# Kernel optimization log

Hardware: AMD Instinct MI355X
Metric: run time of the kernel (lower is better)

The kernel has to match this reference:

```python
import math
import jax, jax.numpy as jnp
import numpy as np

INPUT_DIM = 1024
OUTPUT_DIM = 1024
DEGREE = 8
EPS = 1.0


def setup_inputs() -> dict:
    key = jax.random.key(0)
    k1, k2 = jax.random.split(key)
    x = jax.random.normal(k1, (8192, INPUT_DIM), dtype=jnp.float32)
    std = 1.0 / (INPUT_DIM * (DEGREE + 1))
    hermite_coeffs = std * jax.random.normal(k2, (INPUT_DIM, OUTPUT_DIM, DEGREE + 1), dtype=jnp.float32)
    return {"x": x, "hermite_coeffs": hermite_coeffs}


def _hermite_basis(x):
    # x: [B, I] squashed input; returns [B, I, DEGREE+1] Hermite-function basis.
    pi_q = math.pi ** (-0.25)
    gauss = jnp.exp(-0.5 * x * x)
    h0 = pi_q * gauss
    hs = [h0]
    if DEGREE > 0:
        hs.append(math.sqrt(2.0) * pi_q * x * gauss)
    for i in range(2, DEGREE + 1):
        hs.append(math.sqrt(2.0 / i) * x * hs[i - 1] - math.sqrt((i - 1) / i) * hs[i - 2])
    return jnp.stack(hs, axis=-1)


def reference(x, hermite_coeffs):
    x = x.reshape(-1, INPUT_DIM)
    x = jnp.tanh(x) * (math.sqrt(2 * DEGREE + 1) + EPS)
    hermite = _hermite_basis(x)  # [B, I, D+1]
    y = jnp.einsum('bid,iod->bo', hermite, hermite_coeffs)
    return y.reshape(-1, OUTPUT_DIM)
```

## Files before the change

kernel.cpp:

```cpp
#include <hip/hip_runtime.h>

#define MDIM 8192
#define IDIM 1024
#define ODIM 1024
#define D1   9
#define KDIM (IDIM * D1)

typedef _Float16 half8   __attribute__((ext_vector_type(8)));
typedef _Float16 half2v  __attribute__((ext_vector_type(2)));
typedef float    float4v __attribute__((ext_vector_type(4)));

#define BSCALE 256.0f
#define INV_BSCALE (1.0f / 256.0f)
#define USCALE 5.123105625617661f
#define H0C 0.7511255444649425f
#define SQRT2 1.4142135623730951f

__device__ __forceinline__ void hermite9(float xv, float h[D1]) {
    float ax = fabsf(xv);
    float t  = __expf(-2.0f * ax);
    float th = (1.0f - t) / (1.0f + t);
    th = copysignf(th, xv);
    float u = th * USCALE;
    float g = __expf(-0.5f * u * u);
    h[0] = H0C * g;
    h[1] = SQRT2 * H0C * u * g;
    const float c1[D1] = {0.f, 0.f, 1.0f, 0.8164965809277260f, 0.7071067811865476f,
                          0.6324555320336759f, 0.5773502691896258f, 0.5345224838248488f, 0.5f};
    const float c2[D1] = {0.f, 0.f, 0.7071067811865476f, 0.8164965809277260f, 0.8660254037844386f,
                          0.8944271909999159f, 0.9128709291752769f, 0.9258200997725514f, 0.9354143466934853f};
#pragma unroll
    for (int d = 2; d < D1; ++d) h[d] = c1[d] * u * h[d - 1] - c2[d] * h[d - 2];
}

__global__ __launch_bounds__(256) void prep_b(const float* __restrict__ C,
                                              _Float16* __restrict__ Bt) {
    __shared__ float lds[288 * 33];
    const int t  = threadIdx.x;
    const int ti = blockIdx.x & 31;
    const int to = blockIdx.x >> 5;
    const float* base = C + (size_t)ti * 32 * 9216 + (size_t)to * 32 * 9;
#pragma unroll
    for (int j = 0; j < 36; ++j) {
        int f   = t + 256 * j;
        int row = f / 288;
        int col = f - row * 288;
        lds[col * 33 + row] = base[(size_t)row * 9216 + col];
    }
    __syncthreads();
    _Float16* bb = Bt + (size_t)to * 32 * KDIM + ti * 32;
#pragma unroll
    for (int j = 0; j < 36; ++j) {
        int e   = t + 256 * j;
        int i   = e & 31;
        int odp = e >> 5;
        int ol  = odp / 9;
        int d   = odp - ol * 9;
        bb[(size_t)ol * KDIM + d * IDIM + i] = (_Float16)(lds[odp * 33 + i] * BSCALE);
    }
}

__global__ __launch_bounds__(256) void prep_u(const float* __restrict__ x,
                                              _Float16* __restrict__ U,
                                              _Float16* __restrict__ H0) {
    size_t t = (size_t)blockIdx.x * 256 + threadIdx.x;
    const float4* xp = (const float4*)(x + t * 8);
    float4 a0 = xp[0], a1 = xp[1];
    float xv[8] = {a0.x, a0.y, a0.z, a0.w, a1.x, a1.y, a1.z, a1.w};
    half8 uu, hh;
#pragma unroll
    for (int e = 0; e < 8; ++e) {
        float v  = xv[e];
        float t2 = __expf(-2.0f * fabsf(v));
        float th = (1.0f - t2) / (1.0f + t2);
        float u  = copysignf(th, v) * USCALE;
        float g  = __expf(-0.5f * u * u);
        uu[e] = (_Float16)u;
        hh[e] = (_Float16)(H0C * g);
    }
    *(half8*)(U  + t * 8) = uu;
    *(half8*)(H0 + t * 8) = hh;
}

__global__ __launch_bounds__(256, 2) void gemm_fused2(
    const _Float16* __restrict__ U,
    const _Float16* __restrict__ H0,
    const _Float16* __restrict__ Bt,
    float* __restrict__ out)
{
    const int tid = threadIdx.x;
    const int w = tid >> 6;
    const int l = tid & 63;
    const int bn = blockIdx.x;
    const int bm = blockIdx.y;

    __shared__ _Float16 As[2][128 * 64];
    __shared__ _Float16 Bs[2][128 * 64];

    const int lrow8 = l >> 3;
    const int kgrp  = (l & 7) ^ lrow8;
    const _Float16* Bg = Bt + ((size_t)(bn * 128 + w * 8 + lrow8) * KDIM + kgrp * 8);

    const int q   = l >> 4;
    const int m16 = l & 15;
    const int s3  = m16 & 7;
    const int wm  = w >> 1, wn = w & 1;

    const int r  = tid >> 1;
    const int ih = tid & 1;
    const int r7 = r & 7;
    const size_t urow = (((size_t)(bm * 128 + r)) << 10) + ih * 32;

    constexpr float c1a[D1] = {0.f, 0.f, 1.0f, 0.8164965809277260f, 0.7071067811865476f,
                               0.6324555320336759f, 0.5773502691896258f, 0.5345224838248488f, 0.5f};
    constexpr float c2a[D1] = {0.f, 0.f, 0.7071067811865476f, 0.8164965809277260f, 0.8660254037844386f,
                               0.8944271909999159f, 0.9128709291752769f, 0.9258200997725514f, 0.9354143466934853f};

    half2v u2[16], hA[16], hB[16];
    const half2v sq2 = half2v{(_Float16)SQRT2, (_Float16)SQRT2};

    auto loadUH = [&](int kb) {
        const half8* up = (const half8*)(U  + urow + kb);
        const half8* hp = (const half8*)(H0 + urow + kb);
        half8 ub[4], hb[4];
#pragma unroll
        for (int a = 0; a < 4; ++a) { ub[a] = up[a]; hb[a] = hp[a]; }
#pragma unroll
        for (int a = 0; a < 4; ++a)
#pragma unroll
            for (int b = 0; b < 4; ++b) {
                u2[4*a+b] = half2v{ub[a][2*b], ub[a][2*b+1]};
                hA[4*a+b] = half2v{hb[a][2*b], hb[a][2*b+1]};
            }
#pragma unroll
        for (int p = 0; p < 16; ++p) hB[p] = sq2 * u2[p] * hA[p];
    };

    _Float16* arow0 = &As[0][r * 64];
    _Float16* arow1 = &As[1][r * 64];
    auto writeA = [&](int buf, const half2v ht[16]) {
        _Float16* arow = buf ? arow1 : arow0;
#pragma unroll
        for (int c = 0; c < 4; ++c) {
            int slot = (ih * 4 + c) ^ r7;
            half8 vv;
#pragma unroll
            for (int pp = 0; pp < 4; ++pp) {
                vv[2*pp+0] = ht[4*c+pp][0];
                vv[2*pp+1] = ht[4*c+pp][1];
            }
            *(half8*)(arow + slot * 8) = vv;
        }
    };

    float4v acc[4][4] = {};

#pragma unroll
    for (int rr = 0; rr < 4; ++rr)
        __builtin_amdgcn_global_load_lds(
            (const __attribute__((address_space(1))) void*)(Bg + (size_t)(rr * 32) * KDIM),
            (__attribute__((address_space(3))) void*)((char*)&Bs[0][0] + (rr * 4 + w) * 1024),
            16, 0, 0);
    loadUH(0);
    writeA(0, hA);
    __syncthreads();

    for (int ib = 0; ib < 16; ++ib) {
        const int kbase = ib * 64;
#pragma unroll
        for (int d = 0; d < D1; ++d) {
            const int cur = (ib + d) & 1;
            const int nxt = cur ^ 1;
            const bool has_next = (d < 8) || (ib < 15);

            if (has_next) {
                const int nkoff = (d == 8) ? (kbase + 64)
                                           : ((d + 1) * IDIM + kbase);
#pragma unroll
                for (int rr = 0; rr < 4; ++rr)
                    __builtin_amdgcn_global_load_lds(
                        (const __attribute__((address_space(1))) void*)(Bg + (size_t)(rr * 32) * KDIM + nkoff),
                        (__attribute__((address_space(3))) void*)((char*)&Bs[nxt][0] + (rr * 4 + w) * 1024),
                        16, 0, 0);
            }

            half2v ht[16];
            if (has_next) {
                if (d == 8) {
                    loadUH(kbase + 64);
#pragma unroll
                    for (int p = 0; p < 16; ++p) ht[p] = hA[p];
                } else if (d == 0) {
#pragma unroll
                    for (int p = 0; p < 16; ++p) ht[p] = hB[p];
                } else {
                    const half2v c1v = half2v{(_Float16)c1a[d+1], (_Float16)c1a[d+1]};
                    const half2v c2v = half2v{(_Float16)c2a[d+1], (_Float16)c2a[d+1]};
#pragma unroll
                    for (int p = 0; p < 16; ++p) {
                        half2v t = u2[p] * hB[p];
                        ht[p] = c1v * t - c2v * hA[p];
                        hA[p] = hB[p];
                        hB[p] = ht[p];
                    }
                }
            }

#pragma unroll
            for (int ko = 0; ko < 2; ++ko) {
                const int slot = (q + 4 * ko) ^ s3;
                half8 af[4], bf[4];
#pragma unroll
                for (int i = 0; i < 4; ++i) {
                    af[i] = *(const half8*)&As[cur][(wm * 64 + i * 16 + m16) * 64 + slot * 8];
                    bf[i] = *(const half8*)&Bs[cur][(wn * 64 + i * 16 + m16) * 64 + slot * 8];
                }
#pragma unroll
                for (int i = 0; i < 4; ++i)
#pragma unroll
                    for (int j = 0; j < 4; ++j)
                        acc[i][j] = __builtin_amdgcn_mfma_f32_16x16x32_f16(af[i], bf[j], acc[i][j], 0, 0, 0);
            }

            if (has_next) writeA(nxt, ht);

            __syncthreads();
        }
    }

#pragma unroll
    for (int i = 0; i < 4; ++i) {
        int row = bm * 128 + wm * 64 + i * 16 + q * 4;
#pragma unroll
        for (int j = 0; j < 4; ++j) {
            int col = bn * 128 + wn * 64 + j * 16 + m16;
            float* op = out + (size_t)row * ODIM + col;
#pragma unroll
            for (int r2 = 0; r2 < 4; ++r2)
                op[(size_t)r2 * ODIM] = acc[i][j][r2] * INV_BSCALE;
        }
    }
}

__global__ void naive_kernel(const float* __restrict__ x, const float* __restrict__ C,
                             float* __restrict__ out) {
    __shared__ float hb[IDIM * D1];
    int b = blockIdx.x;
    int tid = threadIdx.x;
    for (int i = tid; i < IDIM; i += 256) {
        float h[D1];
        hermite9(x[(size_t)b * IDIM + i], h);
#pragma unroll
        for (int d = 0; d < D1; ++d) hb[i * D1 + d] = h[d];
    }
    __syncthreads();
    for (int o = tid; o < ODIM; o += 256) {
        float acc = 0.f;
        for (int i = 0; i < IDIM; ++i) {
            const float* cp = C + ((size_t)i * ODIM + o) * D1;
            const float* hp = hb + i * D1;
#pragma unroll
            for (int d = 0; d < D1; ++d) acc += hp[d] * cp[d];
        }
        out[(size_t)b * ODIM + o] = acc;
    }
}

extern "C" void kernel_launch(void* const* d_in, const int* in_sizes, int n_in,
                              void* d_out, int out_size, void* d_ws, size_t ws_size,
                              hipStream_t stream) {
    const float* x      = (const float*)d_in[0];
    const float* coeffs = (const float*)d_in[1];
    float* out = (float*)d_out;

    const size_t bt_bytes = (size_t)ODIM * KDIM * sizeof(_Float16);
    const size_t u_bytes  = (size_t)MDIM * IDIM * sizeof(_Float16);

    if (ws_size >= bt_bytes + 2 * u_bytes) {
        _Float16* Bt = (_Float16*)d_ws;
        _Float16* Uv = (_Float16*)((char*)d_ws + bt_bytes);
        _Float16* H0 = (_Float16*)((char*)d_ws + bt_bytes + u_bytes);
        hipLaunchKernelGGL(prep_b, dim3(1024), dim3(256), 0, stream, coeffs, Bt);
        hipLaunchKernelGGL(prep_u, dim3((MDIM * IDIM) / 2048), dim3(256), 0, stream, x, Uv, H0);
        hipLaunchKernelGGL(gemm_fused2, dim3(8, 64), dim3(256), 0, stream, Uv, H0, Bt, out);
    } else {
        hipLaunchKernelGGL(naive_kernel, dim3(MDIM), dim3(256), 0, stream, x, coeffs, out);
    }
}
```

Before: 281.1 us.

## Generate Hermite A-fragments in registers per wave and merge prep kernels

The GEMM no longer builds the Hermite A tile in shared memory. Each wave loads U and H0 straight into its MFMA fragment layout and runs the recurrence in registers as packed half8 ops, which removes the A LDS writes and reads and halves LDS use. The two prep kernels are merged into one launch, and the tanh divide becomes a reciprocal. In exchange, each wave recomputes the recurrence for its 64 rows (done twice across wn waves), reads U/H0 redundantly from global, and uses more registers, which may limit occupancy.

```diff
diff --git a/kernel.cpp b/kernel.cpp
--- a/kernel.cpp
+++ b/kernel.cpp
@@ -7,7 +7,6 @@
 #define KDIM (IDIM * D1)
 
 typedef _Float16 half8   __attribute__((ext_vector_type(8)));
-typedef _Float16 half2v  __attribute__((ext_vector_type(2)));
 typedef float    float4v __attribute__((ext_vector_type(4)));
 
 #define BSCALE 256.0f
@@ -15,6 +14,11 @@
 #define USCALE 5.123105625617661f
 #define H0C 0.7511255444649425f
 #define SQRT2 1.4142135623730951f
+
+__device__ __forceinline__ half8 splat8(float f) {
+    _Float16 h = (_Float16)f;
+    return half8{h, h, h, h, h, h, h, h};
+}
 
 __device__ __forceinline__ void hermite9(float xv, float h[D1]) {
     float ax = fabsf(xv);
@@ -33,56 +37,57 @@
     for (int d = 2; d < D1; ++d) h[d] = c1[d] * u * h[d - 1] - c2[d] * h[d - 2];
 }
 
-__global__ __launch_bounds__(256) void prep_b(const float* __restrict__ C,
-                                              _Float16* __restrict__ Bt) {
-    __shared__ float lds[288 * 33];
-    const int t  = threadIdx.x;
-    const int ti = blockIdx.x & 31;
-    const int to = blockIdx.x >> 5;
-    const float* base = C + (size_t)ti * 32 * 9216 + (size_t)to * 32 * 9;
-#pragma unroll
-    for (int j = 0; j < 36; ++j) {
-        int f   = t + 256 * j;
-        int row = f / 288;
-        int col = f - row * 288;
-        lds[col * 33 + row] = base[(size_t)row * 9216 + col];
-    }
-    __syncthreads();
-    _Float16* bb = Bt + (size_t)to * 32 * KDIM + ti * 32;
-#pragma unroll
-    for (int j = 0; j < 36; ++j) {
-        int e   = t + 256 * j;
-        int i   = e & 31;
-        int odp = e >> 5;
-        int ol  = odp / 9;
-        int d   = odp - ol * 9;
-        bb[(size_t)ol * KDIM + d * IDIM + i] = (_Float16)(lds[odp * 33 + i] * BSCALE);
-    }
-}
-
-__global__ __launch_bounds__(256) void prep_u(const float* __restrict__ x,
-                                              _Float16* __restrict__ U,
-                                              _Float16* __restrict__ H0) {
-    size_t t = (size_t)blockIdx.x * 256 + threadIdx.x;
-    const float4* xp = (const float4*)(x + t * 8);
-    float4 a0 = xp[0], a1 = xp[1];
-    float xv[8] = {a0.x, a0.y, a0.z, a0.w, a1.x, a1.y, a1.z, a1.w};
-    half8 uu, hh;
-#pragma unroll
-    for (int e = 0; e < 8; ++e) {
-        float v  = xv[e];
-        float t2 = __expf(-2.0f * fabsf(v));
-        float th = (1.0f - t2) / (1.0f + t2);
-        float u  = copysignf(th, v) * USCALE;
-        float g  = __expf(-0.5f * u * u);
-        uu[e] = (_Float16)u;
-        hh[e] = (_Float16)(H0C * g);
-    }
-    *(half8*)(U  + t * 8) = uu;
-    *(half8*)(H0 + t * 8) = hh;
-}
-
-__global__ __launch_bounds__(256, 2) void gemm_fused2(
+__global__ __launch_bounds__(256) void prep_all(const float* __restrict__ C,
+                                                _Float16* __restrict__ Bt,
+                                                const float* __restrict__ x,
+                                                _Float16* __restrict__ U,
+                                                _Float16* __restrict__ H0) {
+    if (blockIdx.x < 1024) {
+        __shared__ float lds[288 * 33];
+        const int t  = threadIdx.x;
+        const int ti = blockIdx.x & 31;
+        const int to = blockIdx.x >> 5;
+        const float* base = C + (size_t)ti * 32 * 9216 + (size_t)to * 32 * 9;
+#pragma unroll
+        for (int j = 0; j < 36; ++j) {
+            int f   = t + 256 * j;
+            int row = f / 288;
+            int col = f - row * 288;
+            lds[col * 33 + row] = base[(size_t)row * 9216 + col];
+        }
+        __syncthreads();
+        _Float16* bb = Bt + (size_t)to * 32 * KDIM + ti * 32;
+#pragma unroll
+        for (int j = 0; j < 36; ++j) {
+            int e   = t + 256 * j;
+            int i   = e & 31;
+            int odp = e >> 5;
+            int ol  = odp / 9;
+            int d   = odp - ol * 9;
+            bb[(size_t)ol * KDIM + d * IDIM + i] = (_Float16)(lds[odp * 33 + i] * BSCALE);
+        }
+    } else {
+        size_t t = (size_t)(blockIdx.x - 1024) * 256 + threadIdx.x;
+        const float4* xp = (const float4*)(x + t * 8);
+        float4 a0 = xp[0], a1 = xp[1];
+        float xv[8] = {a0.x, a0.y, a0.z, a0.w, a1.x, a1.y, a1.z, a1.w};
+        half8 uu, hh;
+#pragma unroll
+        for (int e = 0; e < 8; ++e) {
+            float v  = xv[e];
+            float t2 = __expf(-2.0f * fabsf(v));
+            float th = (1.0f - t2) * __builtin_amdgcn_rcpf(1.0f + t2);
+            float u  = copysignf(th, v) * USCALE;
+            float g  = __expf(-0.5f * u * u);
+            uu[e] = (_Float16)u;
+            hh[e] = (_Float16)(H0C * g);
+        }
+        *(half8*)(U  + t * 8) = uu;
+        *(half8*)(H0 + t * 8) = hh;
+    }
+}
+
+__global__ __launch_bounds__(256, 2) void gemm_fused3(
     const _Float16* __restrict__ U,
     const _Float16* __restrict__ H0,
     const _Float16* __restrict__ Bt,
@@ -94,7 +99,6 @@
     const int bn = blockIdx.x;
     const int bm = blockIdx.y;
 
-    __shared__ _Float16 As[2][128 * 64];
     __shared__ _Float16 Bs[2][128 * 64];
 
     const int lrow8 = l >> 3;
@@ -106,54 +110,29 @@
     const int s3  = m16 & 7;
     const int wm  = w >> 1, wn = w & 1;
 
-    const int r  = tid >> 1;
-    const int ih = tid & 1;
-    const int r7 = r & 7;
-    const size_t urow = (((size_t)(bm * 128 + r)) << 10) + ih * 32;
+    half8 u2[4][2], hA[4][2], hB[4][2];
+    const size_t arow = ((size_t)(bm * 128 + wm * 64 + m16)) << 10;
+    const _Float16* Ubase = U  + arow + 8 * q;
+    const _Float16* Hbase = H0 + arow + 8 * q;
+
+    auto loadUH = [&](int kb) {
+#pragma unroll
+        for (int i = 0; i < 4; ++i)
+#pragma unroll
+            for (int ko = 0; ko < 2; ++ko) {
+                size_t off = ((size_t)(i * 16) << 10) + kb + 32 * ko;
+                u2[i][ko] = *(const half8*)(Ubase + off);
+                hA[i][ko] = *(const half8*)(Hbase + off);
+            }
+    };
+
+    float4v acc[4][4] = {};
+    const half8 sq2v = splat8(SQRT2);
 
     constexpr float c1a[D1] = {0.f, 0.f, 1.0f, 0.8164965809277260f, 0.7071067811865476f,
                                0.6324555320336759f, 0.5773502691896258f, 0.5345224838248488f, 0.5f};
     constexpr float c2a[D1] = {0.f, 0.f, 0.7071067811865476f, 0.8164965809277260f, 0.8660254037844386f,
                                0.8944271909999159f, 0.9128709291752769f, 0.9258200997725514f, 0.9354143466934853f};
-
-    half2v u2[16], hA[16], hB[16];
-    const half2v sq2 = half2v{(_Float16)SQRT2, (_Float16)SQRT2};
-
-    auto loadUH = [&](int kb) {
-        const half8* up = (const half8*)(U  + urow + kb);
-        const half8* hp = (const half8*)(H0 + urow + kb);
-        half8 ub[4], hb[4];
-#pragma unroll
-        for (int a = 0; a < 4; ++a) { ub[a] = up[a]; hb[a] = hp[a]; }
-#pragma unroll
-        for (int a = 0; a < 4; ++a)
-#pragma unroll
-            for (int b = 0; b < 4; ++b) {
-                u2[4*a+b] = half2v{ub[a][2*b], ub[a][2*b+1]};
-                hA[4*a+b] = half2v{hb[a][2*b], hb[a][2*b+1]};
-            }
-#pragma unroll
-        for (int p = 0; p < 16; ++p) hB[p] = sq2 * u2[p] * hA[p];
-    };
-
-    _Float16* arow0 = &As[0][r * 64];
-    _Float16* arow1 = &As[1][r * 64];
-    auto writeA = [&](int buf, const half2v ht[16]) {
-        _Float16* arow = buf ? arow1 : arow0;
-#pragma unroll
-        for (int c = 0; c < 4; ++c) {
-            int slot = (ih * 4 + c) ^ r7;
-            half8 vv;
-#pragma unroll
-            for (int pp = 0; pp < 4; ++pp) {
-                vv[2*pp+0] = ht[4*c+pp][0];
-                vv[2*pp+1] = ht[4*c+pp][1];
-            }
-            *(half8*)(arow + slot * 8) = vv;
-        }
-    };
-
-    float4v acc[4][4] = {};
 
 #pragma unroll
     for (int rr = 0; rr < 4; ++rr)
@@ -162,8 +141,6 @@
             (__attribute__((address_space(3))) void*)((char*)&Bs[0][0] + (rr * 4 + w) * 1024),
             16, 0, 0);
     loadUH(0);
-    writeA(0, hA);
-    __syncthreads();
 
     for (int ib = 0; ib < 16; ++ib) {
         const int kbase = ib * 64;
@@ -171,11 +148,12 @@
         for (int d = 0; d < D1; ++d) {
             const int cur = (ib + d) & 1;
             const int nxt = cur ^ 1;
+
+            __syncthreads();
+
             const bool has_next = (d < 8) || (ib < 15);
-
             if (has_next) {
-                const int nkoff = (d == 8) ? (kbase + 64)
-                                           : ((d + 1) * IDIM + kbase);
+                const int nkoff = (d == 8) ? (kbase + 64) : ((d + 1) * IDIM + kbase);
 #pragma unroll
                 for (int rr = 0; rr < 4; ++rr)
                     __builtin_amdgcn_global_load_lds(
@@ -184,47 +162,59 @@
                         16, 0, 0);
             }
 
-            half2v ht[16];
-            if (has_next) {
-                if (d == 8) {
-                    loadUH(kbase + 64);
-#pragma unroll
-                    for (int p = 0; p < 16; ++p) ht[p] = hA[p];
-                } else if (d == 0) {
-#pragma unroll
-                    for (int p = 0; p < 16; ++p) ht[p] = hB[p];
-                } else {
-                    const half2v c1v = half2v{(_Float16)c1a[d+1], (_Float16)c1a[d+1]};
-                    const half2v c2v = half2v{(_Float16)c2a[d+1], (_Float16)c2a[d+1]};
-#pragma unroll
-                    for (int p = 0; p < 16; ++p) {
-                        half2v t = u2[p] * hB[p];
-                        ht[p] = c1v * t - c2v * hA[p];
-                        hA[p] = hB[p];
-                        hB[p] = ht[p];
+            half8 af[4][2];
+            if (d == 0) {
+#pragma unroll
+                for (int i = 0; i < 4; ++i)
+#pragma unroll
+                    for (int ko = 0; ko < 2; ++ko) {
+                        hB[i][ko] = sq2v * u2[i][ko] * hA[i][ko];
+                        af[i][ko] = hA[i][ko];
                     }
-                }
+            } else if (d == 1) {
+#pragma unroll
+                for (int i = 0; i < 4; ++i)
+#pragma unroll
+                    for (int ko = 0; ko < 2; ++ko) af[i][ko] = hB[i][ko];
+            } else if (d < 8) {
+                const half8 c1v = splat8(c1a[d]);
+                const half8 c2v = splat8(c2a[d]);
+#pragma unroll
+                for (int i = 0; i < 4; ++i)
+#pragma unroll
+                    for (int ko = 0; ko < 2; ++ko) {
+                        half8 t  = u2[i][ko] * hB[i][ko];
+                        half8 ht = c1v * t - c2v * hA[i][ko];
+                        hA[i][ko] = hB[i][ko];
+                        hB[i][ko] = ht;
+                        af[i][ko] = ht;
+                    }
+            } else {
+                const half8 c1v = splat8(c1a[8]);
+                const half8 c2v = splat8(c2a[8]);
+#pragma unroll
+                for (int i = 0; i < 4; ++i)
+#pragma unroll
+                    for (int ko = 0; ko < 2; ++ko) {
+                        half8 t = u2[i][ko] * hB[i][ko];
+                        af[i][ko] = c1v * t - c2v * hA[i][ko];
+                    }
+                if (ib < 15) loadUH(kbase + 64);
             }
 
 #pragma unroll
             for (int ko = 0; ko < 2; ++ko) {
                 const int slot = (q + 4 * ko) ^ s3;
-                half8 af[4], bf[4];
-#pragma unroll
-                for (int i = 0; i < 4; ++i) {
-                    af[i] = *(const half8*)&As[cur][(wm * 64 + i * 16 + m16) * 64 + slot * 8];
-                    bf[i] = *(const half8*)&Bs[cur][(wn * 64 + i * 16 + m16) * 64 + slot * 8];
-                }
+                half8 bf[4];
+#pragma unroll
+                for (int j = 0; j < 4; ++j)
+                    bf[j] = *(const half8*)&Bs[cur][(wn * 64 + j * 16 + m16) * 64 + slot * 8];
 #pragma unroll
                 for (int i = 0; i < 4; ++i)
 #pragma unroll
                     for (int j = 0; j < 4; ++j)
-                        acc[i][j] = __builtin_amdgcn_mfma_f32_16x16x32_f16(af[i], bf[j], acc[i][j], 0, 0, 0);
-            }
-
-            if (has_next) writeA(nxt, ht);
-
-            __syncthreads();
+                        acc[i][j] = __builtin_amdgcn_mfma_f32_16x16x32_f16(af[i][ko], bf[j], acc[i][j], 0, 0, 0);
+            }
         }
     }
 
@@ -280,9 +270,9 @@
         _Float16* Bt = (_Float16*)d_ws;
         _Float16* Uv = (_Float16*)((char*)d_ws + bt_bytes);
         _Float16* H0 = (_Float16*)((char*)d_ws + bt_bytes + u_bytes);
-        hipLaunchKernelGGL(prep_b, dim3(1024), dim3(256), 0, stream, coeffs, Bt);
-        hipLaunchKernelGGL(prep_u, dim3((MDIM * IDIM) / 2048), dim3(256), 0, stream, x, Uv, H0);
-        hipLaunchKernelGGL(gemm_fused2, dim3(8, 64), dim3(256), 0, stream, Uv, H0, Bt, out);
+        hipLaunchKernelGGL(prep_all, dim3(1024 + (MDIM * IDIM) / 2048), dim3(256), 0, stream,
+                           coeffs, Bt, x, Uv, H0);
+        hipLaunchKernelGGL(gemm_fused3, dim3(8, 64), dim3(256), 0, stream, Uv, H0, Bt, out);
     } else {
         hipLaunchKernelGGL(naive_kernel, dim3(MDIM), dim3(256), 0, stream, x, coeffs, out);
     }
```

After: 284.8 us. About the same (+1.3%).
